# Performance work log

Hardware: AMD Instinct MI355X
Metric: run time of the kernel (lower is better)

Reference implementation:

```python
import jax, jax.numpy as jnp
import numpy as np

B, L, H, HS, OUT = 4, 512, 768, 64, 16  # batch, seq_len, hidden, head_size, output_size


def setup_inputs() -> dict:
    key = jax.random.key(0)
    ks = jax.random.split(key, 4)
    return {
        "x": jax.random.normal(ks[0], (B, L, H), dtype=jnp.float32),
        "Wq": jax.random.normal(ks[1], (H, HS), dtype=jnp.float32) * 0.02,
        "bq": jnp.zeros((HS,), dtype=jnp.float32),
        "Wk": jax.random.normal(ks[2], (H, HS), dtype=jnp.float32) * 0.02,
        "bk": jnp.zeros((HS,), dtype=jnp.float32),
        "Wb": jax.random.normal(ks[3], (4 * HS, OUT), dtype=jnp.float32) * 0.02,
        "bb": jnp.zeros((OUT,), dtype=jnp.float32),
    }


def _tri_indices(seq_len):
    # pair p corresponds to (start=i, end=j) with j >= i, ordered by i then j
    idx_start = np.repeat(np.arange(seq_len), np.arange(seq_len, 0, -1))
    idx_end = np.concatenate([np.arange(i, seq_len) for i in range(seq_len)])
    return idx_start, idx_end


def reference(x, Wq, bq, Wk, bk, Wb, bb):
    seq_len = x.shape[1]
    idx_start, idx_end = _tri_indices(seq_len)  # static numpy, P = L*(L+1)/2

    # Project per-token first (math-equivalent to projecting the gathered
    # pair tensors, since Linear is applied token-wise), then gather pairs.
    q = x @ Wq + bq  # [B, L, HS]
    k = x @ Wk + bk  # [B, L, HS]

    q_start = q[:, idx_start]  # query(start_token_hidden)  [B, P, HS]
    q_end = q[:, idx_end]      # query(end_token_hidden)
    k_end = k[:, idx_end]      # key(end_token_hidden) == key_start == key_end

    # entity_type_bias(cat([query_start, key_start, query_end, key_end]))
    feat = jnp.concatenate([q_start, k_end, q_end, k_end], axis=-1) @ Wb + bb  # [B, P, OUT]

    # einsum('blnh,blnh->bln') with n=1 -> per-pair dot product, broadcast over OUT
    score = jnp.einsum('bph,bph->bp', q_start, k_end)[..., None]  # [B, P, 1]
    return score + feat  # [B, P, OUT]
```

## Files before the change

kernel.cpp:

```cpp
#include <hip/hip_runtime.h>
#include <hip/hip_bf16.h>

#define Bc   4
#define Lc   512
#define Hc   768
#define HSc  64
#define OUTc 16
#define Pc   131328
#define KSEG 192

typedef float floatx4 __attribute__((ext_vector_type(4)));


__global__ __launch_bounds__(512, 4) void qk_proj_kernel(
    const float* __restrict__ x,
    const float* __restrict__ Wq, const float* __restrict__ bq,
    const float* __restrict__ Wk, const float* __restrict__ bk,
    const float* __restrict__ Wb, const float* __restrict__ bb,
    float* __restrict__ qws, float* __restrict__ kws,
    float* __restrict__ Aws, float* __restrict__ Ews)
{
    __shared__ float lds_p[4][4][128];
    __shared__ float lds_c[4][128];

    const int tid = threadIdx.x;
    const int wu  = __builtin_amdgcn_readfirstlane(tid >> 6);
    const int half = wu & 1;
    const int kseg = wu >> 1;
    const int col  = tid & 63;
    const int tok_base = blockIdx.x * 4;

    const float* Wp = half ? Wk : Wq;
    const float* wp = Wp + (size_t)kseg * KSEG * HSc + col;
    const float* xr = x + (size_t)tok_base * Hc + kseg * KSEG;

    float acc0 = 0.f, acc1 = 0.f, acc2 = 0.f, acc3 = 0.f;
    float wA[16], wB[16];

    #pragma unroll
    for (int u = 0; u < 16; ++u) wA[u] = wp[u * HSc];

    #pragma unroll 1
    for (int j0 = 0; j0 < KSEG; j0 += 32) {
        #pragma unroll
        for (int u = 0; u < 16; ++u) wB[u] = wp[(j0 + 16 + u) * HSc];
        #pragma unroll
        for (int u = 0; u < 16; ++u) {
            const int jj = j0 + u;
            const float x0 = xr[jj];
            const float x1 = xr[Hc + jj];
            const float x2 = xr[2 * Hc + jj];
            const float x3 = xr[3 * Hc + jj];
            acc0 += x0 * wA[u];
            acc1 += x1 * wA[u];
            acc2 += x2 * wA[u];
            acc3 += x3 * wA[u];
        }
        if (j0 + 32 < KSEG) {
            #pragma unroll
            for (int u = 0; u < 16; ++u) wA[u] = wp[(j0 + 32 + u) * HSc];
        }
        #pragma unroll
        for (int u = 0; u < 16; ++u) {
            const int jj = j0 + 16 + u;
            const float x0 = xr[jj];
            const float x1 = xr[Hc + jj];
            const float x2 = xr[2 * Hc + jj];
            const float x3 = xr[3 * Hc + jj];
            acc0 += x0 * wB[u];
            acc1 += x1 * wB[u];
            acc2 += x2 * wB[u];
            acc3 += x3 * wB[u];
        }
    }

    const int n = half * 64 + col;
    lds_p[kseg][0][n] = acc0;
    lds_p[kseg][1][n] = acc1;
    lds_p[kseg][2][n] = acc2;
    lds_p[kseg][3][n] = acc3;
    __syncthreads();

    if (tid < 512) {
        const int t = tid >> 7;
        const int c = tid & 127;
        float v = lds_p[0][t][c] + lds_p[1][t][c] + lds_p[2][t][c] + lds_p[3][t][c];
        const int cc = c & 63;
        if (c < 64) { v += bq[cc]; qws[(size_t)(tok_base + t) * HSc + cc] = v; }
        else        { v += bk[cc]; kws[(size_t)(tok_base + t) * HSc + cc] = v; }
        lds_c[t][c] = v;
    }
    __syncthreads();

    if (tid < 128) {
        const int t = tid >> 5;
        const int c = tid & 31;
        const int tok = tok_base + t;
        const float* row = lds_c[t];
        if (c < 16) {
            float a = 0.f;
            #pragma unroll 8
            for (int h = 0; h < 64; ++h)
                a += row[h] * Wb[h * OUTc + c];
            Aws[(size_t)tok * OUTc + c] = a;
        } else {
            const int o = c - 16;
            float ev = bb[o];
            #pragma unroll 8
            for (int h = 0; h < 64; ++h) {
                ev += row[h]      * Wb[(128 + h) * OUTc + o];
                ev += row[64 + h] * (Wb[(64 + h) * OUTc + o] + Wb[(192 + h) * OUTc + o]);
            }
            Ews[(size_t)tok * OUTc + o] = ev;
        }
    }
}

__global__ __launch_bounds__(256) void pair_kernel(
    const float* __restrict__ qws, const float* __restrict__ kws,
    const float* __restrict__ Aws, const float* __restrict__ Ews,
    float* __restrict__ out)
{
    __shared__ alignas(16) float lds_q[2][HSc];
    __shared__ alignas(16) float lds_A[2][OUTc];

    const int j = blockIdx.x;
    const int b = blockIdx.y;
    const int s1 = j;
    const int s2 = Lc - 1 - j;
    const int n1 = Lc - s1;

    const int tid = threadIdx.x;
    if (tid < 64) {
        lds_q[0][tid] = qws[((size_t)b * Lc + s1) * HSc + tid];
    } else if (tid < 128) {
        lds_q[1][tid - 64] = qws[((size_t)b * Lc + s2) * HSc + (tid - 64)];
    } else if (tid < 144) {
        lds_A[0][tid - 128] = Aws[((size_t)b * Lc + s1) * OUTc + (tid - 128)];
    } else if (tid < 160) {
        lds_A[1][tid - 144] = Ews[0] * 0.f + Aws[((size_t)b * Lc + s2) * OUTc + (tid - 144)];
    }
    __syncthreads();

    const int P1 = s1 * (2 * Lc + 1 - s1) / 2;
    const int P2 = s2 * (2 * Lc + 1 - s2) / 2;
    const int lane = tid & 3;
    const int slot = tid >> 2;

    const float* kb = kws + (size_t)b * Lc * HSc;
    const float* Eb = Ews + (size_t)b * Lc * OUTc;
    float* ob = out + (size_t)b * Pc * OUTc;

    auto do_pair = [&](int p) {
        const int which = (p < n1) ? 0 : 1;
        const int e   = which ? (s2 + (p - n1)) : (s1 + p);
        const int row = which ? (P2 + (p - n1)) : (P1 + p);

        const float4* kk = (const float4*)(kb + (size_t)e * HSc);
        const float4* qq = (const float4*)lds_q[which];

        float4 kv0 = kk[lane];
        float4 kv1 = kk[4 + lane];
        float4 kv2 = kk[8 + lane];
        float4 kv3 = kk[12 + lane];
        const float4 ev = ((const float4*)(Eb + (size_t)e * OUTc))[lane];

        float4 qv0 = qq[lane];
        float4 qv1 = qq[4 + lane];
        float4 qv2 = qq[8 + lane];
        float4 qv3 = qq[12 + lane];

        float sc = qv0.x * kv0.x + qv0.y * kv0.y + qv0.z * kv0.z + qv0.w * kv0.w;
        sc += qv1.x * kv1.x + qv1.y * kv1.y + qv1.z * kv1.z + qv1.w * kv1.w;
        sc += qv2.x * kv2.x + qv2.y * kv2.y + qv2.z * kv2.z + qv2.w * kv2.w;
        sc += qv3.x * kv3.x + qv3.y * kv3.y + qv3.z * kv3.z + qv3.w * kv3.w;
        sc += __shfl_xor(sc, 1);
        sc += __shfl_xor(sc, 2);

        const float4 av = ((const float4*)lds_A[which])[lane];
        floatx4 r;
        r.x = av.x + ev.x + sc;
        r.y = av.y + ev.y + sc;
        r.z = av.z + ev.z + sc;
        r.w = av.w + ev.w + sc;
        __builtin_nontemporal_store(r, (floatx4*)(ob + (size_t)row * OUTc) + lane);
    };

    #pragma unroll
    for (int i = 0; i < 4; ++i) {
        do_pair(slot + 128 * i);
        do_pair(slot + 128 * i + 64);
    }
    if (slot == 0) do_pair(512);
}

extern "C" void kernel_launch(void* const* d_in, const int* in_sizes, int n_in,
                              void* d_out, int out_size, void* d_ws, size_t ws_size,
                              hipStream_t stream) {
    const float* x  = (const float*)d_in[0];
    const float* Wq = (const float*)d_in[1];
    const float* bq = (const float*)d_in[2];
    const float* Wk = (const float*)d_in[3];
    const float* bk = (const float*)d_in[4];
    const float* Wb = (const float*)d_in[5];
    const float* bb = (const float*)d_in[6];

    float* ws  = (float*)d_ws;
    float* qws = ws;
    float* kws = ws + 131072;
    float* Aws = ws + 262144;
    float* Ews = ws + 294912;

    qk_proj_kernel<<<dim3(512), dim3(512), 0, stream>>>(
        x, Wq, bq, Wk, bk, Wb, bb, qws, kws, Aws, Ews);
    pair_kernel<<<dim3(256, 4), dim3(256), 0, stream>>>(
        qws, kws, Aws, Ews, (float*)d_out);
}
```

Measured before the change: 100.2 us.

## Tile pair kernel over start/end token blocks and widen projection to 8 tokens

```diff
diff --git a/kernel.cpp b/kernel.cpp
--- a/kernel.cpp
+++ b/kernel.cpp
@@ -8,11 +8,12 @@
 #define OUTc 16
 #define Pc   131328
 #define KSEG 192
+#define MTOK 8
 
 typedef float floatx4 __attribute__((ext_vector_type(4)));
 
 
-__global__ __launch_bounds__(512, 4) void qk_proj_kernel(
+__global__ __launch_bounds__(512) void qk_proj_kernel(
     const float* __restrict__ x,
     const float* __restrict__ Wq, const float* __restrict__ bq,
     const float* __restrict__ Wk, const float* __restrict__ bk,
@@ -20,23 +21,25 @@
     float* __restrict__ qws, float* __restrict__ kws,
     float* __restrict__ Aws, float* __restrict__ Ews)
 {
-    __shared__ float lds_p[4][4][128];
-    __shared__ float lds_c[4][128];
+    __shared__ float lds_p[4][MTOK][128];
+    __shared__ float lds_c[MTOK][128];
 
     const int tid = threadIdx.x;
     const int wu  = __builtin_amdgcn_readfirstlane(tid >> 6);
     const int half = wu & 1;
     const int kseg = wu >> 1;
     const int col  = tid & 63;
-    const int tok_base = blockIdx.x * 4;
+    const int tok_base = blockIdx.x * MTOK;
 
     const float* Wp = half ? Wk : Wq;
     const float* wp = Wp + (size_t)kseg * KSEG * HSc + col;
     const float* xr = x + (size_t)tok_base * Hc + kseg * KSEG;
 
-    float acc0 = 0.f, acc1 = 0.f, acc2 = 0.f, acc3 = 0.f;
+    float acc[MTOK];
+    #pragma unroll
+    for (int t = 0; t < MTOK; ++t) acc[t] = 0.f;
+
     float wA[16], wB[16];
-
     #pragma unroll
     for (int u = 0; u < 16; ++u) wA[u] = wp[u * HSc];
 
@@ -47,14 +50,9 @@
         #pragma unroll
         for (int u = 0; u < 16; ++u) {
             const int jj = j0 + u;
-            const float x0 = xr[jj];
-            const float x1 = xr[Hc + jj];
-            const float x2 = xr[2 * Hc + jj];
-            const float x3 = xr[3 * Hc + jj];
-            acc0 += x0 * wA[u];
-            acc1 += x1 * wA[u];
-            acc2 += x2 * wA[u];
-            acc3 += x3 * wA[u];
+            #pragma unroll
+            for (int t = 0; t < MTOK; ++t)
+                acc[t] += xr[t * Hc + jj] * wA[u];
         }
         if (j0 + 32 < KSEG) {
             #pragma unroll
@@ -63,27 +61,21 @@
         #pragma unroll
         for (int u = 0; u < 16; ++u) {
             const int jj = j0 + 16 + u;
-            const float x0 = xr[jj];
-            const float x1 = xr[Hc + jj];
-            const float x2 = xr[2 * Hc + jj];
-            const float x3 = xr[3 * Hc + jj];
-            acc0 += x0 * wB[u];
-            acc1 += x1 * wB[u];
-            acc2 += x2 * wB[u];
-            acc3 += x3 * wB[u];
+            #pragma unroll
+            for (int t = 0; t < MTOK; ++t)
+                acc[t] += xr[t * Hc + jj] * wB[u];
         }
     }
 
     const int n = half * 64 + col;
-    lds_p[kseg][0][n] = acc0;
-    lds_p[kseg][1][n] = acc1;
-    lds_p[kseg][2][n] = acc2;
-    lds_p[kseg][3][n] = acc3;
+    #pragma unroll
+    for (int t = 0; t < MTOK; ++t) lds_p[kseg][t][n] = acc[t];
     __syncthreads();
 
-    if (tid < 512) {
-        const int t = tid >> 7;
-        const int c = tid & 127;
+    #pragma unroll
+    for (int i = tid; i < MTOK * 128; i += 512) {
+        const int t = i >> 7;
+        const int c = i & 127;
         float v = lds_p[0][t][c] + lds_p[1][t][c] + lds_p[2][t][c] + lds_p[3][t][c];
         const int cc = c & 63;
         if (c < 64) { v += bq[cc]; qws[(size_t)(tok_base + t) * HSc + cc] = v; }
@@ -92,7 +84,7 @@
     }
     __syncthreads();
 
-    if (tid < 128) {
+    if (tid < MTOK * 32) {
         const int t = tid >> 5;
         const int c = tid & 31;
         const int tok = tok_base + t;
@@ -121,77 +113,70 @@
     const float* __restrict__ Aws, const float* __restrict__ Ews,
     float* __restrict__ out)
 {
-    __shared__ alignas(16) float lds_q[2][HSc];
-    __shared__ alignas(16) float lds_A[2][OUTc];
-
     const int j = blockIdx.x;
-    const int b = blockIdx.y;
-    const int s1 = j;
-    const int s2 = Lc - 1 - j;
-    const int n1 = Lc - s1;
+    const int i = blockIdx.y;
+    const int b = blockIdx.z;
+    if (j < (i >> 2)) return;
+
+    __shared__ alignas(16) float q_tile[16][64];
+    __shared__ alignas(16) float A_tile[16][16];
 
     const int tid = threadIdx.x;
-    if (tid < 64) {
-        lds_q[0][tid] = qws[((size_t)b * Lc + s1) * HSc + tid];
-    } else if (tid < 128) {
-        lds_q[1][tid - 64] = qws[((size_t)b * Lc + s2) * HSc + (tid - 64)];
-    } else if (tid < 144) {
-        lds_A[0][tid - 128] = Aws[((size_t)b * Lc + s1) * OUTc + (tid - 128)];
-    } else if (tid < 160) {
-        lds_A[1][tid - 144] = Ews[0] * 0.f + Aws[((size_t)b * Lc + s2) * OUTc + (tid - 144)];
+    const int s0 = i * 16;
+    const int e0 = j * 64;
+
+    {
+        const int r = tid >> 4, c4 = tid & 15;
+        ((float4*)q_tile[r])[c4] =
+            ((const float4*)(qws + ((size_t)b * Lc + s0 + r) * HSc))[c4];
+        if (tid < 64) {
+            const int ra = tid >> 2, ca = tid & 3;
+            ((float4*)A_tile[ra])[ca] =
+                ((const float4*)(Aws + ((size_t)b * Lc + s0 + ra) * OUTc))[ca];
+        }
     }
     __syncthreads();
 
-    const int P1 = s1 * (2 * Lc + 1 - s1) / 2;
-    const int P2 = s2 * (2 * Lc + 1 - s2) / 2;
-    const int lane = tid & 3;
-    const int slot = tid >> 2;
-
-    const float* kb = kws + (size_t)b * Lc * HSc;
-    const float* Eb = Ews + (size_t)b * Lc * OUTc;
+    const int g = tid >> 2;
+    const int l = tid & 3;
+    const int e = e0 + g;
+
+    const float4* kk = (const float4*)(kws + ((size_t)b * Lc + e) * HSc);
+    const float4 kv0 = kk[l];
+    const float4 kv1 = kk[4 + l];
+    const float4 kv2 = kk[8 + l];
+    const float4 kv3 = kk[12 + l];
+    const float4 ev  = ((const float4*)(Ews + ((size_t)b * Lc + e) * OUTc))[l];
+
     float* ob = out + (size_t)b * Pc * OUTc;
 
-    auto do_pair = [&](int p) {
-        const int which = (p < n1) ? 0 : 1;
-        const int e   = which ? (s2 + (p - n1)) : (s1 + p);
-        const int row = which ? (P2 + (p - n1)) : (P1 + p);
-
-        const float4* kk = (const float4*)(kb + (size_t)e * HSc);
-        const float4* qq = (const float4*)lds_q[which];
-
-        float4 kv0 = kk[lane];
-        float4 kv1 = kk[4 + lane];
-        float4 kv2 = kk[8 + lane];
-        float4 kv3 = kk[12 + lane];
-        const float4 ev = ((const float4*)(Eb + (size_t)e * OUTc))[lane];
-
-        float4 qv0 = qq[lane];
-        float4 qv1 = qq[4 + lane];
-        float4 qv2 = qq[8 + lane];
-        float4 qv3 = qq[12 + lane];
-
-        float sc = qv0.x * kv0.x + qv0.y * kv0.y + qv0.z * kv0.z + qv0.w * kv0.w;
-        sc += qv1.x * kv1.x + qv1.y * kv1.y + qv1.z * kv1.z + qv1.w * kv1.w;
-        sc += qv2.x * kv2.x + qv2.y * kv2.y + qv2.z * kv2.z + qv2.w * kv2.w;
-        sc += qv3.x * kv3.x + qv3.y * kv3.y + qv3.z * kv3.z + qv3.w * kv3.w;
+    #pragma unroll 4
+    for (int sl = 0; sl < 16; ++sl) {
+        const int s = s0 + sl;
+        const float4* qq = (const float4*)q_tile[sl];
+        const float4 qv0 = qq[l];
+        const float4 qv1 = qq[4 + l];
+        const float4 qv2 = qq[8 + l];
+        const float4 qv3 = qq[12 + l];
+
+        float sc = qv0.x * kv0.x + qv0.y * kv0.y + qv0.z * kv0.z + qv0.w * kv0.w
+                 + qv1.x * kv1.x + qv1.y * kv1.y + qv1.z * kv1.z + qv1.w * kv1.w
+                 + qv2.x * kv2.x + qv2.y * kv2.y + qv2.z * kv2.z + qv2.w * kv2.w
+                 + qv3.x * kv3.x + qv3.y * kv3.y + qv3.z * kv3.z + qv3.w * kv3.w;
         sc += __shfl_xor(sc, 1);
         sc += __shfl_xor(sc, 2);
 
-        const float4 av = ((const float4*)lds_A[which])[lane];
-        floatx4 r;
-        r.x = av.x + ev.x + sc;
-        r.y = av.y + ev.y + sc;
-        r.z = av.z + ev.z + sc;
-        r.w = av.w + ev.w + sc;
-        __builtin_nontemporal_store(r, (floatx4*)(ob + (size_t)row * OUTc) + lane);
-    };
-
-    #pragma unroll
-    for (int i = 0; i < 4; ++i) {
-        do_pair(slot + 128 * i);
-        do_pair(slot + 128 * i + 64);
-    }
-    if (slot == 0) do_pair(512);
+        if (e >= s) {
+            const float4 av = ((const float4*)A_tile[sl])[l];
+            const int row = s * (2 * Lc + 1 - s) / 2 + (e - s);
+            floatx4 r;
+            r.x = av.x + ev.x + sc;
+            r.y = av.y + ev.y + sc;
+            r.z = av.z + ev.z + sc;
+            r.w = av.w + ev.w + sc;
+            __builtin_nontemporal_store(r, (floatx4*)(ob + (size_t)row * OUTc) + l);
+        }
+    }
 }
 
 extern "C" void kernel_launch(void* const* d_in, const int* in_sizes, int n_in,
@@ -211,8 +196,8 @@
     float* Aws = ws + 262144;
     float* Ews = ws + 294912;
 
-    qk_proj_kernel<<<dim3(512), dim3(512), 0, stream>>>(
+    qk_proj_kernel<<<dim3(256), dim3(512), 0, stream>>>(
         x, Wq, bq, Wk, bk, Wb, bb, qws, kws, Aws, Ews);
-    pair_kernel<<<dim3(256, 4), dim3(256), 0, stream>>>(
+    pair_kernel<<<dim3(8, 32, 4), dim3(256), 0, stream>>>(
         qws, kws, Aws, Ews, (float*)d_out);
 }
```

After: 108.8 us. 1.09x slower.
